# Kernel optimization log

Measured on AMD Instinct MI355X. Metric: run time of the kernel, lower is better.

The kernel has to match this reference:

```python
import jax, jax.numpy as jnp
import numpy as np

N_TOKENS = 262144
IN_DIM = 512
NUM_EXPERTS = 64
D_E = 64
TOP_K = 2
EPS = 1e-12  # torch F.normalize eps


def _l2norm(x, axis):
    n = jnp.linalg.norm(x, axis=axis, keepdims=True)
    return x / jnp.maximum(n, EPS)


def setup_inputs() -> dict:
    key = jax.random.key(0)
    k_h, k_w, k_e, k_svd = jax.random.split(key, 4)
    h = jax.random.normal(k_h, (N_TOKENS, IN_DIM), dtype=jnp.float32)
    # xavier_uniform for W [d_e, in_dim]
    limit = float(np.sqrt(6.0 / (D_E + IN_DIM)))
    W = jax.random.uniform(k_w, (D_E, IN_DIM), minval=-limit, maxval=limit, dtype=jnp.float32)
    # orthonormal expert embeddings (SVD of random matrix), scaled by init_expert_norm=0.1
    M = jax.random.normal(k_svd, (D_E, D_E), dtype=jnp.float32)
    U, _, _ = jnp.linalg.svd(M)
    expert_embeddings = U[:NUM_EXPERTS, :] * 0.1
    tau = jnp.array(1.0, dtype=jnp.float32)
    return {"h": h, "W": W, "expert_embeddings": expert_embeddings, "tau": tau}


def reference(h, W, expert_embeddings, tau):
    # projection: [N, d_e]
    h_proj = h @ W.T
    h_norm = _l2norm(h_proj, axis=1)
    e_norm = _l2norm(expert_embeddings, axis=1)
    # cosine scores: [N, E]
    scores = h_norm @ e_norm.T
    full_gates = jax.nn.softmax(scores / tau, axis=1)
    topk_values, topk_indices = jax.lax.top_k(full_gates, TOP_K)
    normalized_topk = jax.nn.softmax(topk_values, axis=1)
    rows = jnp.arange(full_gates.shape[0])[:, None]
    sparse_gates = jnp.zeros_like(full_gates).at[rows, topk_indices].set(normalized_topk)
    return sparse_gates, topk_indices, full_gates
```

## Files before the change

kernel.cpp:

```cpp
#include <hip/hip_runtime.h>
#include <hip/hip_fp16.h>
#include <math.h>

#define NT 262144
#define KD 512
#define NE 64
#define DE 64

constexpr int BM = 128;
constexpr int NS = KD / 32;
constexpr int WS_EN = 32768;
constexpr int LD2 = 68;
constexpr float RSC  = 4096.0f;
constexpr float IRSC = 1.0f / 4096.0f;

using f32x4 = __attribute__((ext_vector_type(4))) float;
using f16x8 = __attribute__((ext_vector_type(8))) _Float16;

typedef const __attribute__((address_space(1))) unsigned int* gp1_t;
typedef __attribute__((address_space(3))) unsigned int* lp3_t;

__device__ __forceinline__ void splitf16(float4 lo, float4 hi,
                                         f16x8& o1, f16x8& o2) {
    float x[8] = {lo.x, lo.y, lo.z, lo.w, hi.x, hi.y, hi.z, hi.w};
    union { unsigned int u[4]; f16x8 v; } r1, r2;
    #pragma unroll
    for (int p = 0; p < 4; ++p) {
        float f0 = x[2 * p], f1 = x[2 * p + 1];
        __half2 h1 = __float22half2_rn(make_float2(f0, f1));
        float2 bk = __half22float2(h1);
        __half2 h2 = __float22half2_rn(make_float2((f0 - bk.x) * RSC,
                                                   (f1 - bk.y) * RSC));
        r1.u[p] = *reinterpret_cast<unsigned int*>(&h1);
        r2.u[p] = *reinterpret_cast<unsigned int*>(&h2);
    }
    o1 = r1.v; o2 = r2.v;
}

__device__ __forceinline__ f16x8 ld_frag(const unsigned int* p) {
    union { uint4 q; f16x8 v; } u;
    u.q = *(const uint4*)p;
    return u.v;
}

__global__ void prep(const float* __restrict__ W, const float* __restrict__ E,
                     unsigned int* __restrict__ ws) {
    const int tid = threadIdx.x;
    if (blockIdx.x < 16) {
        const int idx = blockIdx.x * 256 + tid;
        const int row = idx >> 6, k8 = idx & 63;
        const float* src = W + (size_t)row * KD + k8 * 8;
        float4 lo = *(const float4*)src, hi = *(const float4*)(src + 4);
        f16x8 o1, o2;
        splitf16(lo, hi, o1, o2);
        union { f16x8 v; uint4 q; } u1, u2;
        u1.v = o1; u2.v = o2;
        const int ks = k8 >> 2, lk = k8 & 3, ct = row >> 4, lr = row & 15;
        const int g = ks * 4 + ct, lane = lk * 16 + lr;
        unsigned int* base = ws + (size_t)g * 512 + lane * 4;
        *(uint4*)(base)       = u1.q;
        *(uint4*)(base + 256) = u2.q;
    } else {
        const int er = tid >> 2, part = tid & 3;
        float ss = 0.f;
        float4 ev[4];
        #pragma unroll
        for (int u = 0; u < 4; ++u) {
            ev[u] = *(const float4*)(E + er * DE + part * 16 + u * 4);
            ss = fmaf(ev[u].x, ev[u].x, ss);
            ss = fmaf(ev[u].y, ev[u].y, ss);
            ss = fmaf(ev[u].z, ev[u].z, ss);
            ss = fmaf(ev[u].w, ev[u].w, ss);
        }
        ss += __shfl_xor(ss, 1, 64);
        ss += __shfl_xor(ss, 2, 64);
        const float inv_e = 1.0f / fmaxf(sqrtf(ss), 1e-12f);
        #pragma unroll
        for (int u = 0; u < 4; ++u) {
            ev[u].x *= inv_e; ev[u].y *= inv_e; ev[u].z *= inv_e; ev[u].w *= inv_e;
        }
        #pragma unroll
        for (int half = 0; half < 2; ++half) {
            const int d0 = part * 16 + half * 8;
            f16x8 o1, o2;
            splitf16(ev[half * 2], ev[half * 2 + 1], o1, o2);
            union { f16x8 v; uint4 q; } u1, u2;
            u1.v = o1; u2.v = o2;
            const int k2 = d0 >> 5, kg = (d0 >> 3) & 3;
            const int ge = k2 * 4 + (er >> 4), l = (er & 15) | (kg << 4);
            unsigned int* base = ws + WS_EN + (size_t)ge * 512 + l * 4;
            *(uint4*)(base)       = u1.q;
            *(uint4*)(base + 256) = u2.q;
        }
    }
}

__global__ __launch_bounds__(256, 4) void moe_all(const float* __restrict__ h,
                                                  const unsigned int* __restrict__ wsW,
                                                  const float* __restrict__ tau_p,
                                                  float* __restrict__ out) {
    __shared__ float smem[8704];

    const int tid = threadIdx.x;
    const int lane = tid & 63;
    const int wv = tid >> 6;
    const int lr = lane & 15;
    const int lk = lane >> 4;
    const long tok0 = (long)blockIdx.x * BM;

    f32x4 acc[2][4], ac2[2][4];
    #pragma unroll
    for (int rt = 0; rt < 2; ++rt)
        #pragma unroll
        for (int ct = 0; ct < 4; ++ct) {
            acc[rt][ct] = (f32x4){0.f, 0.f, 0.f, 0.f};
            ac2[rt][ct] = (f32x4){0.f, 0.f, 0.f, 0.f};
        }

#define STAGE_A(KS)                                                            \
    {                                                                          \
        _Pragma("unroll")                                                      \
        for (int n = 0; n < 4; ++n) {                                          \
            const int flat = (wv * 4 + n) * 64 + lane;                         \
            const int t = flat >> 3, q = flat & 7;                             \
            const int qs = q ^ (t & 7);                                        \
            const float* g = h + (tok0 + t) * (long)KD + (KS) * 32 + qs * 4;   \
            float* l = smem + 4096 + wv * 1024 + n * 256;                      \
            __builtin_amdgcn_global_load_lds((gp1_t)(const void*)g,            \
                                             (lp3_t)(void*)l, 16, 0, 0);       \
        }                                                                      \
    }

#define STAGE_B(CUR, KS)                                                       \
    {                                                                          \
        _Pragma("unroll")                                                      \
        for (int i = 0; i < 2; ++i) {                                          \
            const unsigned int* g = wsW + (size_t)(KS) * 2048 + i * 1024       \
                                    + wv * 256 + lane * 4;                     \
            float* l = smem + (CUR) * 2048 + i * 1024 + wv * 256;              \
            __builtin_amdgcn_global_load_lds((gp1_t)(const void*)g,            \
                                             (lp3_t)(void*)l, 16, 0, 0);       \
        }                                                                      \
    }

    STAGE_B(0, 0);
    STAGE_A(0);

    const int sw = lr & 7;
    const int q0 = (lk * 2) ^ sw;
    const int q1 = (lk * 2 + 1) ^ sw;
    const float* abase = smem + 4096 + wv * 1024;

    for (int ks = 0; ks < NS; ++ks) {
        const int cur = ks & 1;
        asm volatile("s_waitcnt vmcnt(0)" ::: "memory");
        __builtin_amdgcn_s_barrier();
        if (ks + 1 < NS) { STAGE_B(cur ^ 1, ks + 1); }
        __builtin_amdgcn_sched_barrier(0);

        float4 xl0 = *(const float4*)(abase + lr * 32 + q0 * 4);
        float4 xh0 = *(const float4*)(abase + lr * 32 + q1 * 4);
        float4 xl1 = *(const float4*)(abase + (lr + 16) * 32 + q0 * 4);
        float4 xh1 = *(const float4*)(abase + (lr + 16) * 32 + q1 * 4);
        asm volatile("s_waitcnt lgkmcnt(0)" ::: "memory");
        if (ks + 1 < NS) { STAGE_A(ks + 1); }
        __builtin_amdgcn_sched_barrier(0);

        f16x8 a1[2], a2[2];
        splitf16(xl0, xh0, a1[0], a2[0]);
        splitf16(xl1, xh1, a1[1], a2[1]);

        #pragma unroll
        for (int ct = 0; ct < 4; ++ct) {
            const unsigned int* bb =
                (const unsigned int*)(smem + cur * 2048) + ct * 512 + lane * 4;
            f16x8 b1 = ld_frag(bb);
            f16x8 b2 = ld_frag(bb + 256);
            f32x4 c0 = acc[0][ct], c1 = acc[1][ct];
            f32x4 d0 = ac2[0][ct], d1 = ac2[1][ct];
            c0 = __builtin_amdgcn_mfma_f32_16x16x32_f16(a1[0], b1, c0, 0, 0, 0);
            c1 = __builtin_amdgcn_mfma_f32_16x16x32_f16(a1[1], b1, c1, 0, 0, 0);
            d0 = __builtin_amdgcn_mfma_f32_16x16x32_f16(a1[0], b2, d0, 0, 0, 0);
            d1 = __builtin_amdgcn_mfma_f32_16x16x32_f16(a1[1], b2, d1, 0, 0, 0);
            d0 = __builtin_amdgcn_mfma_f32_16x16x32_f16(a2[0], b1, d0, 0, 0, 0);
            d1 = __builtin_amdgcn_mfma_f32_16x16x32_f16(a2[1], b1, d1, 0, 0, 0);
            acc[0][ct] = c0; acc[1][ct] = c1;
            ac2[0][ct] = d0; ac2[1][ct] = d1;
        }
    }

    #pragma unroll
    for (int rt = 0; rt < 2; ++rt)
        #pragma unroll
        for (int ct = 0; ct < 4; ++ct)
            #pragma unroll
            for (int r = 0; r < 4; ++r)
                acc[rt][ct][r] = fmaf(ac2[rt][ct][r], IRSC, acc[rt][ct][r]);

    float inv_n[2][4];
    #pragma unroll
    for (int rt = 0; rt < 2; ++rt) {
        #pragma unroll
        for (int r = 0; r < 4; ++r) {
            float ss = 0.f;
            #pragma unroll
            for (int ct = 0; ct < 4; ++ct)
                ss = fmaf(acc[rt][ct][r], acc[rt][ct][r], ss);
            ss += __shfl_xor(ss, 1, 64);
            ss += __shfl_xor(ss, 2, 64);
            ss += __shfl_xor(ss, 4, 64);
            ss += __shfl_xor(ss, 8, 64);
            inv_n[rt][r] = 1.0f / fmaxf(sqrtf(ss), 1e-12f);
        }
    }

    __syncthreads();

    #pragma unroll
    for (int rt = 0; rt < 2; ++rt)
        #pragma unroll
        for (int ct = 0; ct < 4; ++ct)
            #pragma unroll
            for (int r = 0; r < 4; ++r) {
                const int t = wv * 32 + rt * 16 + lk * 4 + r;
                smem[t * LD2 + ct * 16 + lr] = acc[rt][ct][r] * inv_n[rt][r];
            }

    const unsigned int* wsE = wsW + WS_EN;
    f32x4 sc[2][4], sc2[2][4];
    #pragma unroll
    for (int rt = 0; rt < 2; ++rt)
        #pragma unroll
        for (int ce = 0; ce < 4; ++ce) {
            sc[rt][ce]  = (f32x4){0.f, 0.f, 0.f, 0.f};
            sc2[rt][ce] = (f32x4){0.f, 0.f, 0.f, 0.f};
        }

    #pragma unroll
    for (int k2 = 0; k2 < 2; ++k2) {
        f16x8 ha1[2], ha2[2];
        #pragma unroll
        for (int rt = 0; rt < 2; ++rt) {
            const float* ra = smem + (wv * 32 + rt * 16 + lr) * LD2 + k2 * 32 + lk * 8;
            float4 lo = *(const float4*)ra;
            float4 hi = *(const float4*)(ra + 4);
            splitf16(lo, hi, ha1[rt], ha2[rt]);
        }
        #pragma unroll
        for (int ce = 0; ce < 4; ++ce) {
            const unsigned int* bb = wsE + (k2 * 4 + ce) * 512 + lane * 4;
            f16x8 b1 = ld_frag(bb);
            f16x8 b2 = ld_frag(bb + 256);
            #pragma unroll
            for (int rt = 0; rt < 2; ++rt) {
                f32x4 c = sc[rt][ce], d = sc2[rt][ce];
                c = __builtin_amdgcn_mfma_f32_16x16x32_f16(ha1[rt], b1, c, 0, 0, 0);
                d = __builtin_amdgcn_mfma_f32_16x16x32_f16(ha1[rt], b2, d, 0, 0, 0);
                d = __builtin_amdgcn_mfma_f32_16x16x32_f16(ha2[rt], b1, d, 0, 0, 0);
                sc[rt][ce] = c; sc2[rt][ce] = d;
            }
        }
    }

    const float inv_tau = 1.0f / tau_p[0];
    float* outS = out;
    float* outI = out + (size_t)NT * 64;
    float* outF = out + (size_t)NT * 66;

    #pragma unroll
    for (int rt = 0; rt < 2; ++rt) {
        #pragma unroll
        for (int r = 0; r < 4; ++r) {
            const long tok = tok0 + wv * 32 + rt * 16 + lk * 4 + r;
            float s[4];
            #pragma unroll
            for (int ce = 0; ce < 4; ++ce)
                s[ce] = fmaf(sc2[rt][ce][r], IRSC, sc[rt][ce][r]) * inv_tau;

            unsigned long long k1 = 0ULL, k2 = 0ULL;
            #pragma unroll
            for (int ce = 0; ce < 4; ++ce) {
                unsigned int ou = __float_as_uint(s[ce]);
                ou = (ou & 0x80000000u) ? ~ou : (ou | 0x80000000u);
                unsigned long long key = ((unsigned long long)ou << 6)
                                       | (unsigned long long)(63 - (ce * 16 + lr));
                if (key > k1) { k2 = k1; k1 = key; }
                else if (key > k2) { k2 = key; }
            }
            #pragma unroll
            for (int msk = 1; msk <= 8; msk <<= 1) {
                unsigned long long o1 = __shfl_xor(k1, msk, 64);
                unsigned long long o2 = __shfl_xor(k2, msk, 64);
                unsigned long long hi = k1 > o1 ? k1 : o1;
                unsigned long long lo = k1 > o1 ? o1 : k1;
                unsigned long long m2 = k2 > o2 ? k2 : o2;
                k2 = lo > m2 ? lo : m2;
                k1 = hi;
            }
            const int i1 = 63 - (int)(k1 & 63ULL);
            const int i2 = 63 - (int)(k2 & 63ULL);
            const unsigned int u1 = (unsigned int)(k1 >> 6);
            const unsigned int u2 = (unsigned int)(k2 >> 6);
            const float v1 = __uint_as_float((u1 & 0x80000000u) ? (u1 ^ 0x80000000u) : ~u1);
            const float v2 = __uint_as_float((u2 & 0x80000000u) ? (u2 ^ 0x80000000u) : ~u2);

            const float m = v1;

            float g[4], z = 0.f;
            #pragma unroll
            for (int ce = 0; ce < 4; ++ce) { g[ce] = __expf(s[ce] - m); z += g[ce]; }
            z += __shfl_xor(z, 1, 64);
            z += __shfl_xor(z, 2, 64);
            z += __shfl_xor(z, 4, 64);
            z += __shfl_xor(z, 8, 64);
            const float invZ = 1.0f / z;

            #pragma unroll
            for (int ce = 0; ce < 4; ++ce)
                outF[tok * 64 + ce * 16 + lr] = g[ce] * invZ;

            const float gv1 = invZ;
            const float gv2 = __expf(v2 - m) * invZ;
            const float qq = __expf(gv2 - gv1);
            const float w1 = 1.0f / (1.0f + qq);
            const float w2 = qq * w1;

            #pragma unroll
            for (int ce = 0; ce < 4; ++ce) {
                int e = ce * 16 + lr;
                outS[tok * 64 + e] = (e == i1) ? w1 : ((e == i2) ? w2 : 0.0f);
            }
            if (lr == 0) {
                *(float2*)(outI + tok * 2) = make_float2((float)i1, (float)i2);
            }
        }
    }
#undef STAGE_A
#undef STAGE_B
}

extern "C" void kernel_launch(void* const* d_in, const int* in_sizes, int n_in,
                              void* d_out, int out_size, void* d_ws, size_t ws_size,
                              hipStream_t stream) {
    const float* h   = (const float*)d_in[0];
    const float* W   = (const float*)d_in[1];
    const float* E   = (const float*)d_in[2];
    const float* tau = (const float*)d_in[3];
    float* out = (float*)d_out;
    unsigned int* ws = (unsigned int*)d_ws;

    prep<<<17, 256, 0, stream>>>(W, E, ws);
    moe_all<<<NT / BM, 256, 0, stream>>>(h, ws, tau, out);
}
```

Baseline: 153.4 us.

## Load activation tiles directly into registers with double-buffered prefetch instead of LDS

The h operand used to be staged through LDS with global_load_lds and then read back into registers. It is now loaded straight from global memory into registers, one k-step ahead, using two alternating float4 register sets. The main loop is unrolled by two through a PHASE macro so the current and next buffers swap roles. This removes the LDS write/read round-trip and the lgkmcnt wait for A, at the cost of more VGPRs and less coalesced strided global loads per wave.

```diff
diff --git a/kernel.cpp b/kernel.cpp
--- a/kernel.cpp
+++ b/kernel.cpp
@@ -107,6 +107,7 @@
     const int lr = lane & 15;
     const int lk = lane >> 4;
     const long tok0 = (long)blockIdx.x * BM;
+    const long wtok = tok0 + wv * 32;
 
     f32x4 acc[2][4], ac2[2][4];
     #pragma unroll
@@ -116,20 +117,6 @@
             acc[rt][ct] = (f32x4){0.f, 0.f, 0.f, 0.f};
             ac2[rt][ct] = (f32x4){0.f, 0.f, 0.f, 0.f};
         }
-
-#define STAGE_A(KS)                                                            \
-    {                                                                          \
-        _Pragma("unroll")                                                      \
-        for (int n = 0; n < 4; ++n) {                                          \
-            const int flat = (wv * 4 + n) * 64 + lane;                         \
-            const int t = flat >> 3, q = flat & 7;                             \
-            const int qs = q ^ (t & 7);                                        \
-            const float* g = h + (tok0 + t) * (long)KD + (KS) * 32 + qs * 4;   \
-            float* l = smem + 4096 + wv * 1024 + n * 256;                      \
-            __builtin_amdgcn_global_load_lds((gp1_t)(const void*)g,            \
-                                             (lp3_t)(void*)l, 16, 0, 0);       \
-        }                                                                      \
-    }
 
 #define STAGE_B(CUR, KS)                                                       \
     {                                                                          \
@@ -143,50 +130,51 @@
         }                                                                      \
     }
 
+#define PHASE(CL0, CH0, CL1, CH1, NL0, NH0, NL1, NH1, KS, LAST)                \
+    {                                                                          \
+        asm volatile("s_waitcnt vmcnt(0)" ::: "memory");   \
+        __builtin_amdgcn_s_barrier();            \
+        if (!(LAST)) {                                                         \
+            STAGE_B(((KS) + 1) & 1, (KS) + 1);                                 \
+            const int o = ((KS) + 1) * 32;                                     \
+            NL0 = *(const float4*)(pa0 + o); NH0 = *(const float4*)(pa0 + o + 4); \
+            NL1 = *(const float4*)(pa1 + o); NH1 = *(const float4*)(pa1 + o + 4); \
+        }                                                                      \
+        __builtin_amdgcn_sched_barrier(0);                                     \
+        f16x8 a1[2], a2[2];                                                    \
+        splitf16(CL0, CH0, a1[0], a2[0]);                                      \
+        splitf16(CL1, CH1, a1[1], a2[1]);                                      \
+        _Pragma("unroll")                                                      \
+        for (int ct = 0; ct < 4; ++ct) {                                       \
+            const unsigned int* bb =                                           \
+                (const unsigned int*)(smem + ((KS) & 1) * 2048)                \
+                + ct * 512 + lane * 4;                                         \
+            f16x8 b1 = ld_frag(bb);                                            \
+            f16x8 b2 = ld_frag(bb + 256);                                      \
+            f32x4 c0 = acc[0][ct], c1 = acc[1][ct];                            \
+            f32x4 d0 = ac2[0][ct], d1 = ac2[1][ct];                            \
+            c0 = __builtin_amdgcn_mfma_f32_16x16x32_f16(a1[0], b1, c0, 0, 0, 0); \
+            c1 = __builtin_amdgcn_mfma_f32_16x16x32_f16(a1[1], b1, c1, 0, 0, 0); \
+            d0 = __builtin_amdgcn_mfma_f32_16x16x32_f16(a1[0], b2, d0, 0, 0, 0); \
+            d1 = __builtin_amdgcn_mfma_f32_16x16x32_f16(a1[1], b2, d1, 0, 0, 0); \
+            d0 = __builtin_amdgcn_mfma_f32_16x16x32_f16(a2[0], b1, d0, 0, 0, 0); \
+            d1 = __builtin_amdgcn_mfma_f32_16x16x32_f16(a2[1], b1, d1, 0, 0, 0); \
+            acc[0][ct] = c0; acc[1][ct] = c1;                                  \
+            ac2[0][ct] = d0; ac2[1][ct] = d1;                                  \
+        }                                                                      \
+    }
+
+    const float* pa0 = h + (wtok + 0 * 16 + lr) * (long)KD + lk * 8;
+    const float* pa1 = h + (wtok + 1 * 16 + lr) * (long)KD + lk * 8;
+
     STAGE_B(0, 0);
-    STAGE_A(0);
-
-    const int sw = lr & 7;
-    const int q0 = (lk * 2) ^ sw;
-    const int q1 = (lk * 2 + 1) ^ sw;
-    const float* abase = smem + 4096 + wv * 1024;
-
-    for (int ks = 0; ks < NS; ++ks) {
-        const int cur = ks & 1;
-        asm volatile("s_waitcnt vmcnt(0)" ::: "memory");
-        __builtin_amdgcn_s_barrier();
-        if (ks + 1 < NS) { STAGE_B(cur ^ 1, ks + 1); }
-        __builtin_amdgcn_sched_barrier(0);
-
-        float4 xl0 = *(const float4*)(abase + lr * 32 + q0 * 4);
-        float4 xh0 = *(const float4*)(abase + lr * 32 + q1 * 4);
-        float4 xl1 = *(const float4*)(abase + (lr + 16) * 32 + q0 * 4);
-        float4 xh1 = *(const float4*)(abase + (lr + 16) * 32 + q1 * 4);
-        asm volatile("s_waitcnt lgkmcnt(0)" ::: "memory");
-        if (ks + 1 < NS) { STAGE_A(ks + 1); }
-        __builtin_amdgcn_sched_barrier(0);
-
-        f16x8 a1[2], a2[2];
-        splitf16(xl0, xh0, a1[0], a2[0]);
-        splitf16(xl1, xh1, a1[1], a2[1]);
-
-        #pragma unroll
-        for (int ct = 0; ct < 4; ++ct) {
-            const unsigned int* bb =
-                (const unsigned int*)(smem + cur * 2048) + ct * 512 + lane * 4;
-            f16x8 b1 = ld_frag(bb);
-            f16x8 b2 = ld_frag(bb + 256);
-            f32x4 c0 = acc[0][ct], c1 = acc[1][ct];
-            f32x4 d0 = ac2[0][ct], d1 = ac2[1][ct];
-            c0 = __builtin_amdgcn_mfma_f32_16x16x32_f16(a1[0], b1, c0, 0, 0, 0);
-            c1 = __builtin_amdgcn_mfma_f32_16x16x32_f16(a1[1], b1, c1, 0, 0, 0);
-            d0 = __builtin_amdgcn_mfma_f32_16x16x32_f16(a1[0], b2, d0, 0, 0, 0);
-            d1 = __builtin_amdgcn_mfma_f32_16x16x32_f16(a1[1], b2, d1, 0, 0, 0);
-            d0 = __builtin_amdgcn_mfma_f32_16x16x32_f16(a2[0], b1, d0, 0, 0, 0);
-            d1 = __builtin_amdgcn_mfma_f32_16x16x32_f16(a2[1], b1, d1, 0, 0, 0);
-            acc[0][ct] = c0; acc[1][ct] = c1;
-            ac2[0][ct] = d0; ac2[1][ct] = d1;
-        }
+    float4 xl0 = *(const float4*)(pa0), xh0 = *(const float4*)(pa0 + 4);
+    float4 xl1 = *(const float4*)(pa1), xh1 = *(const float4*)(pa1 + 4);
+    float4 yl0 = xl0, yh0 = xh0, yl1 = xl1, yh1 = xh1;
+
+    for (int ks = 0; ks < NS; ks += 2) {
+        PHASE(xl0, xh0, xl1, xh1, yl0, yh0, yl1, yh1, ks,     0);
+        PHASE(yl0, yh0, yl1, yh1, xl0, xh0, xl1, xh1, ks + 1, (ks + 1 == NS - 1));
     }
 
     #pragma unroll
@@ -335,8 +323,8 @@
             }
         }
     }
-#undef STAGE_A
 #undef STAGE_B
+#undef PHASE
 }
 
 extern "C" void kernel_launch(void* const* d_in, const int* in_sizes, int n_in,
```

Measured after the change: 193.6 us. 1.26x slower.
